# Optimization experiments

Measured on AMD Instinct MI355X. Metric: run time of the kernel, lower is better.

The kernel has to match this reference:

```python
import jax, jax.numpy as jnp
import numpy as np

NUM_EXPERT = 32
IN_FEAT = 256
OUT_FEAT = 256
TOTAL_TOKENS = 524288
CAPACITY = 16896  # static per-expert pad, > max expected count


def setup_inputs() -> dict:
    key = jax.random.key(0)
    k_inp, k_w = jax.random.split(key)
    inp = jax.random.normal(k_inp, (TOTAL_TOKENS, IN_FEAT), dtype=jnp.float32)
    # weight initialized like nn.Linear (kaiming-uniform-ish); scale of randn is fine for a numeric baseline
    weight = jax.random.normal(k_w, (NUM_EXPERT, OUT_FEAT, IN_FEAT), dtype=jnp.float32) * (1.0 / np.sqrt(IN_FEAT))
    # variable-sized expert groups summing exactly to TOTAL_TOKENS (tokens assumed pre-sorted by expert)
    rng = np.random.default_rng(0)
    counts = rng.multinomial(TOTAL_TOKENS, np.ones(NUM_EXPERT) / NUM_EXPERT)
    assert counts.max() <= CAPACITY and counts.sum() == TOTAL_TOKENS
    fwd_expert_count = jnp.asarray(counts, dtype=jnp.int64)
    return {"inp": inp, "weight": weight, "fwd_expert_count": fwd_expert_count, "capacity": CAPACITY}


def reference(inp, weight, fwd_expert_count, capacity):
    # Grouped GEMM: for expert e, out[seg_e] = inp[seg_e] @ weight[e].T
    E = weight.shape[0]
    T = inp.shape[0]
    counts = fwd_expert_count.astype(jnp.int32)
    cum = jnp.cumsum(counts)                       # [E] inclusive prefix sums
    starts = cum - counts                          # [E] segment starts
    tok = jnp.arange(T, dtype=jnp.int32)
    eid = jnp.searchsorted(cum, tok, side='right') # [T] expert id per token
    pos = tok - starts[eid]                        # [T] slot within expert group
    # Scatter tokens into padded per-expert buffer [E, capacity, in]
    buf = jnp.zeros((E, capacity, inp.shape[1]), dtype=inp.dtype).at[eid, pos].set(inp)
    # Batched matmul against per-expert weights [E, out, in] -> [E, capacity, out]
    y = jnp.einsum('eci,eoi->eco', buf, weight)
    # Gather back to token order [T, out]
    return y[eid, pos]
```

## Files before the change

### kernel.cpp

```cpp
#include <hip/hip_runtime.h>
#include <cstdint>
#include <cstddef>

#define NEXPERT 32
#define KIN 256
#define NOUT 256
#define NTOK 524288
#define BM 64

typedef float f32x4 __attribute__((ext_vector_type(4)));
typedef __bf16 bf16x8 __attribute__((ext_vector_type(8)));
typedef unsigned short u16;
typedef u16 u16x8 __attribute__((ext_vector_type(8)));
typedef unsigned int u32;

union BF8 { u16x8 u; bf16x8 b; };

__device__ __forceinline__ u16 f2bf(float f) {
  unsigned u = __float_as_uint(f);
  return (u16)((u + 0x7FFFu + ((u >> 16) & 1u)) >> 16);
}

#define GLDS(gp, lp) __builtin_amdgcn_global_load_lds(                      \
    (const __attribute__((address_space(1))) u32*)(gp),                      \
    (__attribute__((address_space(3))) u32*)(u32)(uintptr_t)(lp), 16, 0, 0)

#define VMW(n) asm volatile("s_waitcnt vmcnt(" n ")" ::: "memory")
#define BAR()  do { __builtin_amdgcn_sched_barrier(0);                       \
                    __builtin_amdgcn_s_barrier();                            \
                    __builtin_amdgcn_sched_barrier(0); } while (0)

__global__ void pack_w_kernel(const float* __restrict__ w, u16* __restrict__ wb) {
  const int t    = blockIdx.x * 256 + threadIdx.x;
  const int lane = t & 63;
  const int n16  = (t >> 6) & 15;
  const int kc   = (t >> 10) & 7;
  const int e    = t >> 13;
  const float* src = w + (size_t)e * 65536 + (size_t)(n16 * 16 + (lane & 15)) * 256
                       + kc * 32 + (lane >> 4) * 8;
  const float4 a = *reinterpret_cast<const float4*>(src);
  const float4 b = *reinterpret_cast<const float4*>(src + 4);
  u16x8 h;
  h[0]=f2bf(a.x); h[1]=f2bf(a.y); h[2]=f2bf(a.z); h[3]=f2bf(a.w);
  h[4]=f2bf(b.x); h[5]=f2bf(b.y); h[6]=f2bf(b.z); h[7]=f2bf(b.w);
  *reinterpret_cast<u16x8*>(wb + (size_t)t * 8) = h;
}

template<bool WSBF>
__device__ __forceinline__ void loadBstep(const u16* wEL, const float* wF,
                                          int wv, int l15, int lg, int s,
                                          BF8 (&d)[2][4]) {
  if (WSBF) {
#pragma unroll
    for (int c = 0; c < 2; ++c)
#pragma unroll
      for (int n = 0; n < 4; ++n)
        d[c][n].u = *reinterpret_cast<const u16x8*>(
            wEL + (size_t)((2 * s + c) * 16 + (wv << 2) + n) * 512);
  } else {
#pragma unroll
    for (int c = 0; c < 2; ++c)
#pragma unroll
      for (int n = 0; n < 4; ++n) {
        const float4* p = reinterpret_cast<const float4*>(
            wF + (size_t)((wv << 6) + (n << 4) + l15) * KIN + (2 * s + c) * 32 + lg * 8);
        const float4 x = p[0], y = p[1];
        u16x8 h;
        h[0]=f2bf(x.x); h[1]=f2bf(x.y); h[2]=f2bf(x.z); h[3]=f2bf(x.w);
        h[4]=f2bf(y.x); h[5]=f2bf(y.y); h[6]=f2bf(y.z); h[7]=f2bf(y.w);
        d[c][n].u = h;
      }
  }
}

__device__ __forceinline__ void computeStep(const char* sAc, int buf, int l15, int lg,
                                            const BF8 (&bfr)[2][4], f32x4 (&acc)[4][4]) {
  const char* abase = sAc + buf * 16384 + l15 * 256;
#pragma unroll
  for (int c = 0; c < 2; ++c) {
    BF8 af[4];
#pragma unroll
    for (int m = 0; m < 4; ++m) {
      const int g0 = (c << 3) + (lg << 1);
      const f32x4 fa = *reinterpret_cast<const f32x4*>(abase + m * 4096 + (((g0    ) ^ l15) << 4));
      const f32x4 fb = *reinterpret_cast<const f32x4*>(abase + m * 4096 + (((g0 + 1) ^ l15) << 4));
      af[m].b[0]=(__bf16)fa[0]; af[m].b[1]=(__bf16)fa[1];
      af[m].b[2]=(__bf16)fa[2]; af[m].b[3]=(__bf16)fa[3];
      af[m].b[4]=(__bf16)fb[0]; af[m].b[5]=(__bf16)fb[1];
      af[m].b[6]=(__bf16)fb[2]; af[m].b[7]=(__bf16)fb[3];
    }
#pragma unroll
    for (int m = 0; m < 4; ++m)
#pragma unroll
      for (int n = 0; n < 4; ++n)
        acc[m][n] = __builtin_amdgcn_mfma_f32_16x16x32_bf16(
            af[m].b, bfr[c][n].b, acc[m][n], 0, 0, 0);
  }
}

template<bool WSBF>
__global__ __launch_bounds__(256, 3)
void moe_gemm_kernel(const float* __restrict__ inp,
                     const float* w32,
                     const u16* __restrict__ wpk,
                     const int* __restrict__ counts,
                     float* __restrict__ out)
{
  __shared__ float sA[3 * 64 * 64];

  const int tid  = threadIdx.x;
  const int lane = tid & 63;
  const int wv   = tid >> 6;
  const int l15  = lane & 15;
  const int lg   = lane >> 4;

  const long long* c64 = reinterpret_cast<const long long*>(counts);
  const long long p0 = c64[0];
  const bool is64 = (p0 >= 0 && p0 < (1ll << 31));
  int c = 0;
  if (lane < 32) c = is64 ? (int)c64[lane] : counts[lane];
#pragma unroll
  for (int d = 1; d < 32; d <<= 1) {
    const int o = __shfl_up(c, d, 64);
    if (lane >= d) c += o;
  }
  const int cum = (lane < 32) ? c : 0x7fffffff;

  const int t0 = blockIdx.x * BM;
  const int t1 = t0 + BM;

  const float* gp[4];
#pragma unroll
  for (int i = 0; i < 4; ++i) {
    const int r = (wv << 4) + (i << 2) + (lane >> 4);
    const int g = (lane & 15) ^ (r & 15);
    gp[i] = inp + (size_t)(t0 + r) * KIN + g * 4;
  }
  char* const sAc   = reinterpret_cast<char*>(sA);
  char* const lbase = sAc + wv * 4096;

  int rb = t0;
  int e  = __popcll(__ballot(cum <= t0));

  while (rb < t1) {
    const int re = min(t1, __shfl(cum, e));
    if (re > rb) {
      const u16*   wEL = wpk + ((size_t)e << 16) + (lane << 3);
      const float* wF  = w32 + ((size_t)e << 16);

      f32x4 acc[4][4];
      const f32x4 zero = {0.f, 0.f, 0.f, 0.f};
#pragma unroll
      for (int m = 0; m < 4; ++m)
#pragma unroll
        for (int n = 0; n < 4; ++n) acc[m][n] = zero;

      BF8 bA[2][4], bB[2][4];

      BAR();
#pragma unroll
      for (int i = 0; i < 4; ++i) GLDS(gp[i] +   0, lbase +     0 + i * 1024);
      loadBstep<WSBF>(wEL, wF, wv, l15, lg, 0, bA);
#pragma unroll
      for (int i = 0; i < 4; ++i) GLDS(gp[i] +  64, lbase + 16384 + i * 1024);

      VMW("12"); BAR();
      loadBstep<WSBF>(wEL, wF, wv, l15, lg, 1, bB);
#pragma unroll
      for (int i = 0; i < 4; ++i) GLDS(gp[i] + 128, lbase + 32768 + i * 1024);
      computeStep(sAc, 0, l15, lg, bA, acc);

      VMW("12"); BAR();
      loadBstep<WSBF>(wEL, wF, wv, l15, lg, 2, bA);
#pragma unroll
      for (int i = 0; i < 4; ++i) GLDS(gp[i] + 192, lbase +     0 + i * 1024);
      computeStep(sAc, 1, l15, lg, bB, acc);

      VMW("12"); BAR();
      loadBstep<WSBF>(wEL, wF, wv, l15, lg, 3, bB);
      computeStep(sAc, 2, l15, lg, bA, acc);

      VMW("8"); BAR();
      computeStep(sAc, 0, l15, lg, bB, acc);

      const bool full = (rb == t0) & (re == t1);
      if (full) {
#pragma unroll
        for (int m = 0; m < 4; ++m) {
          const int rbase = t0 + (m << 4) + (lg << 2);
#pragma unroll
          for (int n = 0; n < 4; ++n) {
            float* op = out + (size_t)rbase * NOUT + (wv << 6) + (n << 4) + l15;
#pragma unroll
            for (int j = 0; j < 4; ++j) op[(size_t)j * NOUT] = acc[m][n][j];
          }
        }
      } else {
#pragma unroll
        for (int m = 0; m < 4; ++m) {
          const int rbase = t0 + (m << 4) + (lg << 2);
#pragma unroll
          for (int n = 0; n < 4; ++n) {
            float* op = out + (size_t)rbase * NOUT + (wv << 6) + (n << 4) + l15;
#pragma unroll
            for (int j = 0; j < 4; ++j) {
              const int rg = rbase + j;
              if (rg >= rb && rg < re) op[(size_t)j * NOUT] = acc[m][n][j];
            }
          }
        }
      }
    }
    rb = re > rb ? re : rb;
    ++e;
  }
}

extern "C" void kernel_launch(void* const* d_in, const int* in_sizes, int n_in,
                              void* d_out, int out_size, void* d_ws, size_t ws_size,
                              hipStream_t stream) {
  const float* inp    = (const float*)d_in[0];
  const float* w      = (const float*)d_in[1];
  const int*   counts = (const int*)d_in[2];
  float*       out    = (float*)d_out;

  const size_t wbytes = (size_t)NEXPERT * NOUT * KIN * 2;
  const bool usews = (ws_size >= wbytes);

  if (usews) {
    u16* wpk = (u16*)d_ws;
    pack_w_kernel<<<1024, 256, 0, stream>>>(w, wpk);
    moe_gemm_kernel<true><<<NTOK / BM, 256, 0, stream>>>(inp, w, wpk, counts, out);
  } else {
    moe_gemm_kernel<false><<<NTOK / BM, 256, 0, stream>>>(inp, w, nullptr, counts, out);
  }
}
```

Before: 265.7 us.

## Add producer wave with flag-based LDS pipeline and persistent multi-tile blocks

```diff
diff --git a/kernel.cpp b/kernel.cpp
--- a/kernel.cpp
+++ b/kernel.cpp
@@ -6,7 +6,8 @@
 #define KIN 256
 #define NOUT 256
 #define NTOK 524288
-#define BM 64
+#define TPB 8
+#define GSTEPS (TPB * 4)
 
 typedef float f32x4 __attribute__((ext_vector_type(4)));
 typedef __bf16 bf16x8 __attribute__((ext_vector_type(8)));
@@ -21,14 +22,16 @@
   return (u16)((u + 0x7FFFu + ((u >> 16) & 1u)) >> 16);
 }
 
+__device__ __forceinline__ void cvt8(const float4& x, const float4& y, BF8& o) {
+  o.u[0]=f2bf(x.x); o.u[1]=f2bf(x.y); o.u[2]=f2bf(x.z); o.u[3]=f2bf(x.w);
+  o.u[4]=f2bf(y.x); o.u[5]=f2bf(y.y); o.u[6]=f2bf(y.z); o.u[7]=f2bf(y.w);
+}
+
 #define GLDS(gp, lp) __builtin_amdgcn_global_load_lds(                      \
     (const __attribute__((address_space(1))) u32*)(gp),                      \
     (__attribute__((address_space(3))) u32*)(u32)(uintptr_t)(lp), 16, 0, 0)
 
 #define VMW(n) asm volatile("s_waitcnt vmcnt(" n ")" ::: "memory")
-#define BAR()  do { __builtin_amdgcn_sched_barrier(0);                       \
-                    __builtin_amdgcn_s_barrier();                            \
-                    __builtin_amdgcn_sched_barrier(0); } while (0)
 
 __global__ void pack_w_kernel(const float* __restrict__ w, u16* __restrict__ wb) {
   const int t    = blockIdx.x * 256 + threadIdx.x;
@@ -64,11 +67,7 @@
       for (int n = 0; n < 4; ++n) {
         const float4* p = reinterpret_cast<const float4*>(
             wF + (size_t)((wv << 6) + (n << 4) + l15) * KIN + (2 * s + c) * 32 + lg * 8);
-        const float4 x = p[0], y = p[1];
-        u16x8 h;
-        h[0]=f2bf(x.x); h[1]=f2bf(x.y); h[2]=f2bf(x.z); h[3]=f2bf(x.w);
-        h[4]=f2bf(y.x); h[5]=f2bf(y.y); h[6]=f2bf(y.z); h[7]=f2bf(y.w);
-        d[c][n].u = h;
+        cvt8(p[0], p[1], d[c][n]);
       }
   }
 }
@@ -99,14 +98,71 @@
 }
 
 template<bool WSBF>
-__global__ __launch_bounds__(256, 3)
+__device__ void redoRun2(const float* __restrict__ inp, const u16* __restrict__ wpk,
+                         const float* w32, int t0, int rb, int re, int e,
+                         float* __restrict__ out, int wv, int l15, int lg, int lane) {
+  const u16*   wEL = wpk + ((size_t)e << 16) + (lane << 3);
+  const float* wF  = w32 + ((size_t)e << 16);
+  f32x4 acc[4][4];
+  const f32x4 zero = {0.f, 0.f, 0.f, 0.f};
+#pragma unroll
+  for (int m = 0; m < 4; ++m)
+#pragma unroll
+    for (int n = 0; n < 4; ++n) acc[m][n] = zero;
+#pragma unroll
+  for (int q = 0; q < 8; ++q) {
+    BF8 bq[4];
+    if (WSBF) {
+#pragma unroll
+      for (int n = 0; n < 4; ++n)
+        bq[n].u = *reinterpret_cast<const u16x8*>(
+            wEL + (size_t)(q * 16 + (wv << 2) + n) * 512);
+    } else {
+#pragma unroll
+      for (int n = 0; n < 4; ++n) {
+        const float4* p = reinterpret_cast<const float4*>(
+            wF + (size_t)((wv << 6) + (n << 4) + l15) * KIN + q * 32 + lg * 8);
+        cvt8(p[0], p[1], bq[n]);
+      }
+    }
+    BF8 af[4];
+#pragma unroll
+    for (int m = 0; m < 4; ++m) {
+      const float* p = inp + (size_t)(t0 + m * 16 + l15) * KIN + q * 32 + lg * 8;
+      cvt8(*reinterpret_cast<const float4*>(p), *reinterpret_cast<const float4*>(p + 4), af[m]);
+    }
+#pragma unroll
+    for (int m = 0; m < 4; ++m)
+#pragma unroll
+      for (int n = 0; n < 4; ++n)
+        acc[m][n] = __builtin_amdgcn_mfma_f32_16x16x32_bf16(
+            af[m].b, bq[n].b, acc[m][n], 0, 0, 0);
+  }
+#pragma unroll
+  for (int m = 0; m < 4; ++m) {
+    const int rbase = t0 + (m << 4) + (lg << 2);
+#pragma unroll
+    for (int n = 0; n < 4; ++n) {
+      float* op = out + (size_t)rbase * NOUT + (wv << 6) + (n << 4) + l15;
+#pragma unroll
+      for (int j = 0; j < 4; ++j) {
+        const int rg = rbase + j;
+        if (rg >= rb && rg < re) op[(size_t)j * NOUT] = acc[m][n][j];
+      }
+    }
+  }
+}
+
+template<bool WSBF>
+__global__ __launch_bounds__(320, 3)
 void moe_gemm_kernel(const float* __restrict__ inp,
                      const float* w32,
                      const u16* __restrict__ wpk,
                      const int* __restrict__ counts,
                      float* __restrict__ out)
 {
-  __shared__ float sA[3 * 64 * 64];
+  __shared__ float sA[4 * 64 * 64];
+  __shared__ int sSync[8];
 
   const int tid  = threadIdx.x;
   const int lane = tid & 63;
@@ -114,6 +170,49 @@
   const int l15  = lane & 15;
   const int lg   = lane >> 4;
 
+  if (tid < 8) sSync[tid] = 0;
+  __syncthreads();
+
+  const int blk0 = blockIdx.x * (64 * TPB);
+  char* const sAc = reinterpret_cast<char*>(sA);
+  volatile int* vf = sSync;
+  volatile int* vd = sSync + 4;
+
+  if (wv == 4) {
+    const char* inp8 = reinterpret_cast<const char*>(inp);
+    const int rowoff = lane >> 4, swz = lane & 15;
+    int P[4];
+#pragma unroll
+    for (int j = 0; j < 4; ++j) {
+      const int rr = j * 4 + rowoff;
+      P[j] = rr * 1024 + ((swz ^ rr) << 4);
+    }
+    auto STAGE = [&](int g) {
+      const char* src = inp8 + ((size_t)(blk0 + (g >> 2) * 64) << 10) + ((g & 3) << 8);
+      char* dst = sAc + ((g & 3) << 14);
+#pragma unroll
+      for (int i = 0; i < 16; ++i)
+        GLDS((const float*)(src + ((size_t)(i >> 2) << 14) + P[i & 3]), dst + i * 1024);
+    };
+
+    STAGE(0); STAGE(1);
+    VMW("16"); asm volatile("" ::: "memory");
+    if (lane == 0) vf[0] = 1;
+    for (int g = 2; g < GSTEPS; ++g) {
+      const int b = g & 3, need = (g >> 2) * 4;
+      while (vd[b] < need) __builtin_amdgcn_s_sleep(2);
+      asm volatile("" ::: "memory");
+      STAGE(g);
+      VMW("32"); asm volatile("" ::: "memory");
+      if (lane == 0) vf[(g - 2) & 3] = g - 1;
+    }
+    VMW("16"); asm volatile("" ::: "memory");
+    if (lane == 0) vf[(GSTEPS - 2) & 3] = GSTEPS - 1;
+    VMW("0");  asm volatile("" ::: "memory");
+    if (lane == 0) vf[(GSTEPS - 1) & 3] = GSTEPS;
+    return;
+  }
+
   const long long* c64 = reinterpret_cast<const long long*>(counts);
   const long long p0 = c64[0];
   const bool is64 = (p0 >= 0 && p0 < (1ll << 31));
@@ -125,94 +224,105 @@
     if (lane >= d) c += o;
   }
   const int cum = (lane < 32) ? c : 0x7fffffff;
-
-  const int t0 = blockIdx.x * BM;
-  const int t1 = t0 + BM;
-
-  const float* gp[4];
-#pragma unroll
-  for (int i = 0; i < 4; ++i) {
-    const int r = (wv << 4) + (i << 2) + (lane >> 4);
-    const int g = (lane & 15) ^ (r & 15);
-    gp[i] = inp + (size_t)(t0 + r) * KIN + g * 4;
-  }
-  char* const sAc   = reinterpret_cast<char*>(sA);
-  char* const lbase = sAc + wv * 4096;
-
-  int rb = t0;
-  int e  = __popcll(__ballot(cum <= t0));
-
-  while (rb < t1) {
-    const int re = min(t1, __shfl(cum, e));
-    if (re > rb) {
-      const u16*   wEL = wpk + ((size_t)e << 16) + (lane << 3);
-      const float* wF  = w32 + ((size_t)e << 16);
-
-      f32x4 acc[4][4];
-      const f32x4 zero = {0.f, 0.f, 0.f, 0.f};
-#pragma unroll
-      for (int m = 0; m < 4; ++m)
-#pragma unroll
-        for (int n = 0; n < 4; ++n) acc[m][n] = zero;
-
-      BF8 bA[2][4], bB[2][4];
-
-      BAR();
-#pragma unroll
-      for (int i = 0; i < 4; ++i) GLDS(gp[i] +   0, lbase +     0 + i * 1024);
-      loadBstep<WSBF>(wEL, wF, wv, l15, lg, 0, bA);
-#pragma unroll
-      for (int i = 0; i < 4; ++i) GLDS(gp[i] +  64, lbase + 16384 + i * 1024);
-
-      VMW("12"); BAR();
-      loadBstep<WSBF>(wEL, wF, wv, l15, lg, 1, bB);
-#pragma unroll
-      for (int i = 0; i < 4; ++i) GLDS(gp[i] + 128, lbase + 32768 + i * 1024);
-      computeStep(sAc, 0, l15, lg, bA, acc);
-
-      VMW("12"); BAR();
-      loadBstep<WSBF>(wEL, wF, wv, l15, lg, 2, bA);
-#pragma unroll
-      for (int i = 0; i < 4; ++i) GLDS(gp[i] + 192, lbase +     0 + i * 1024);
-      computeStep(sAc, 1, l15, lg, bB, acc);
-
-      VMW("12"); BAR();
-      loadBstep<WSBF>(wEL, wF, wv, l15, lg, 3, bB);
-      computeStep(sAc, 2, l15, lg, bA, acc);
-
-      VMW("8"); BAR();
-      computeStep(sAc, 0, l15, lg, bB, acc);
-
-      const bool full = (rb == t0) & (re == t1);
-      if (full) {
-#pragma unroll
-        for (int m = 0; m < 4; ++m) {
-          const int rbase = t0 + (m << 4) + (lg << 2);
-#pragma unroll
-          for (int n = 0; n < 4; ++n) {
-            float* op = out + (size_t)rbase * NOUT + (wv << 6) + (n << 4) + l15;
-#pragma unroll
-            for (int j = 0; j < 4; ++j) op[(size_t)j * NOUT] = acc[m][n][j];
-          }
+  auto cumAt = [&](int i) { return __shfl(cum, i, 64); };
+
+  auto POLL = [&](int g, int s) {
+    while (vf[s] < g + 1) __builtin_amdgcn_s_sleep(1);
+    asm volatile("" ::: "memory");
+    __builtin_amdgcn_sched_barrier(0);
+  };
+  auto DONE = [&](int s) {
+    asm volatile("" ::: "memory");
+    if (lane == 0) atomicAdd(&sSync[4 + s], 1);
+  };
+  auto CVMW8 = [&]() { if (WSBF) { VMW("8"); } else { VMW("0"); } };
+
+  int e = __popcll(__ballot(cum <= blk0));
+  const u16*   wEL = wpk + ((size_t)e << 16) + (lane << 3);
+  const float* wF  = w32 + ((size_t)e << 16);
+  BF8 bA[2][4], bB[2][4];
+  loadBstep<WSBF>(wEL, wF, wv, l15, lg, 0, bA);
+
+  unsigned redo = 0;
+  for (int t = 0; t < TPB; ++t) {
+    const int t0 = blk0 + (t << 6);
+    const int re = min(t0 + 64, cumAt(e));
+    if (re < t0 + 64) redo |= (1u << t);
+
+    f32x4 acc[4][4];
+    const f32x4 zero = {0.f, 0.f, 0.f, 0.f};
+#pragma unroll
+    for (int m = 0; m < 4; ++m)
+#pragma unroll
+      for (int n = 0; n < 4; ++n) acc[m][n] = zero;
+
+    loadBstep<WSBF>(wEL, wF, wv, l15, lg, 1, bB);
+    POLL(4 * t + 0, 0); CVMW8();
+    computeStep(sAc, 0, l15, lg, bA, acc);
+    DONE(0);
+    loadBstep<WSBF>(wEL, wF, wv, l15, lg, 2, bA);
+    POLL(4 * t + 1, 1); CVMW8();
+    computeStep(sAc, 1, l15, lg, bB, acc);
+    DONE(1);
+    loadBstep<WSBF>(wEL, wF, wv, l15, lg, 3, bB);
+    POLL(4 * t + 2, 2); CVMW8();
+    computeStep(sAc, 2, l15, lg, bA, acc);
+    DONE(2);
+    int eN = e;
+    if (t < TPB - 1) {
+      eN = __popcll(__ballot(cum <= t0 + 64));
+      const u16*   wELn = wpk + ((size_t)eN << 16) + (lane << 3);
+      const float* wFn  = w32 + ((size_t)eN << 16);
+      loadBstep<WSBF>(wELn, wFn, wv, l15, lg, 0, bA);
+      POLL(4 * t + 3, 3); CVMW8();
+      computeStep(sAc, 3, l15, lg, bB, acc);
+    } else {
+      POLL(4 * t + 3, 3); VMW("0");
+      computeStep(sAc, 3, l15, lg, bB, acc);
+    }
+    DONE(3);
+
+    if (re == t0 + 64) {
+#pragma unroll
+      for (int m = 0; m < 4; ++m) {
+        const int rbase = t0 + (m << 4) + (lg << 2);
+#pragma unroll
+        for (int n = 0; n < 4; ++n) {
+          float* op = out + (size_t)rbase * NOUT + (wv << 6) + (n << 4) + l15;
+#pragma unroll
+          for (int j = 0; j < 4; ++j) op[(size_t)j * NOUT] = acc[m][n][j];
         }
-      } else {
-#pragma unroll
-        for (int m = 0; m < 4; ++m) {
-          const int rbase = t0 + (m << 4) + (lg << 2);
-#pragma unroll
-          for (int n = 0; n < 4; ++n) {
-            float* op = out + (size_t)rbase * NOUT + (wv << 6) + (n << 4) + l15;
-#pragma unroll
-            for (int j = 0; j < 4; ++j) {
-              const int rg = rbase + j;
-              if (rg >= rb && rg < re) op[(size_t)j * NOUT] = acc[m][n][j];
-            }
-          }
+      }
+    } else {
+#pragma unroll
+      for (int m = 0; m < 4; ++m) {
+        const int rbase = t0 + (m << 4) + (lg << 2);
+#pragma unroll
+        for (int n = 0; n < 4; ++n) {
+          float* op = out + (size_t)rbase * NOUT + (wv << 6) + (n << 4) + l15;
+#pragma unroll
+          for (int j = 0; j < 4; ++j)
+            if (rbase + j < re) op[(size_t)j * NOUT] = acc[m][n][j];
         }
       }
     }
-    rb = re > rb ? re : rb;
-    ++e;
+    e = eN;
+    wEL = wpk + ((size_t)e << 16) + (lane << 3);
+    wF  = w32 + ((size_t)e << 16);
+  }
+
+  while (redo) {
+    const int t = __builtin_ctz(redo); redo &= redo - 1;
+    const int t0 = blk0 + (t << 6), t1 = t0 + 64;
+    int ee = __popcll(__ballot(cum <= t0));
+    int rbX = min(t1, cumAt(ee));
+    while (rbX < t1) {
+      ++ee;
+      const int reX = min(t1, cumAt(ee));
+      if (reX > rbX)
+        redoRun2<WSBF>(inp, wpk, w32, t0, rbX, reX, ee, out, wv, l15, lg, lane);
+      rbX = reX > rbX ? reX : rbX;
+    }
   }
 }
 
@@ -226,12 +336,13 @@
 
   const size_t wbytes = (size_t)NEXPERT * NOUT * KIN * 2;
   const bool usews = (ws_size >= wbytes);
+  const int grid = NTOK / (64 * TPB);
 
   if (usews) {
     u16* wpk = (u16*)d_ws;
     pack_w_kernel<<<1024, 256, 0, stream>>>(w, wpk);
-    moe_gemm_kernel<true><<<NTOK / BM, 256, 0, stream>>>(inp, w, wpk, counts, out);
+    moe_gemm_kernel<true><<<grid, 320, 0, stream>>>(inp, w, wpk, counts, out);
   } else {
-    moe_gemm_kernel<false><<<NTOK / BM, 256, 0, stream>>>(inp, w, nullptr, counts, out);
-  }
-}
+    moe_gemm_kernel<false><<<grid, 320, 0, stream>>>(inp, w, nullptr, counts, out);
+  }
+}
```

Measured after the change: 631.7 us. +137.7%, slower.
